# Kernel optimization log

Measured on AMD Instinct MI355X. Metric: run time of the kernel, lower is better.

## Reference

```python
import jax, jax.numpy as jnp
import numpy as np

N = 100000          # nodes
F_IN = 500          # num_features
HID = 256           # hidden
C = 40              # out_classes
E = 2302585         # ~ N*ln(N)*ec, doubled (both directions) in spar_samp
ALPHA0 = 0.1        # att[0][0] = alpha*(1-alpha)**0


def setup_inputs() -> dict:
    key = jax.random.key(0)
    ks = jax.random.split(key, 8)
    x = jax.random.normal(ks[0], (N, F_IN), dtype=jnp.float32)
    W1 = jax.random.normal(ks[1], (F_IN, HID), dtype=jnp.float32) * (1.0 / np.sqrt(F_IN))
    b1 = jnp.zeros((HID,), dtype=jnp.float32)
    W2 = jax.random.normal(ks[2], (HID, C), dtype=jnp.float32) * (1.0 / np.sqrt(HID))
    b2 = jnp.zeros((C,), dtype=jnp.float32)
    edge_row = jax.random.randint(ks[3], (E,), 0, N, dtype=jnp.int64) if jax.config.jax_enable_x64 else jax.random.randint(ks[3], (E,), 0, N, dtype=jnp.int32)
    edge_col = jax.random.randint(ks[4], (E,), 0, N, dtype=edge_row.dtype)
    # sampled importance weights: deg^{-1/2}*deg^{-1/2}*(M/num_edgess) -> small positive floats
    edge_val = jax.random.uniform(ks[5], (E,), dtype=jnp.float32, minval=0.001, maxval=0.05)
    return {"x": x, "W1": W1, "b1": b1, "W2": W2, "b2": b2,
            "edge_row": edge_row, "edge_col": edge_col, "edge_val": edge_val}


def reference(x, W1, b1, W2, b2, edge_row, edge_col, edge_val):
    # eval mode: dropout is identity
    h = jax.nn.relu(x @ W1 + b1)          # [N, HID]
    h = h @ W2 + b2                       # [N, C]
    # sparse propagation: out[r] += val * h[c]  (scatter-add SpMM)
    msg = edge_val[:, None] * h[edge_col]            # [E, C] gather
    agg = jax.ops.segment_sum(msg, edge_row, num_segments=N)  # [N, C]
    out = h * ALPHA0 + agg
    return jax.nn.log_softmax(out, axis=1)
```

## Files before the change

kernel.cpp:

```cpp
#include <hip/hip_runtime.h>
#include <hip/hip_bf16.h>


#define N_NODES 100000
#define F_IN    500
#define HID     256
#define C_OUT   40
#define ALPHA0  0.1f

#define RPB     128
#define NBUCK   ((N_NODES + RPB - 1) / RPB)
#define NCH     320
#define SCAN_M  (NBUCK * NCH)
#define SCAN_CHUNK 2048
#define NBS     ((SCAN_M + SCAN_CHUNK - 1) / SCAN_CHUNK)

typedef short short8 __attribute__((ext_vector_type(8)));
typedef float f32x4  __attribute__((ext_vector_type(4)));

__device__ __forceinline__ short f2bf(float f) {
  union { float f; unsigned u; } x; x.f = f;
  unsigned r = x.u + 0x7fffu + ((x.u >> 16) & 1u);
  return (short)(r >> 16);
}
__device__ __forceinline__ float bf2f(short s) {
  union { unsigned u; float f; } x; x.u = ((unsigned)(unsigned short)s) << 16;
  return x.f;
}

__device__ __forceinline__ void lbar() {
  asm volatile("s_waitcnt lgkmcnt(0)" ::: "memory");
  __builtin_amdgcn_s_barrier();
}

__global__ __launch_bounds__(256) void k_pack_weights(
    const float* __restrict__ W1, const float* __restrict__ W2,
    short* __restrict__ W1S, short* __restrict__ W2T)
{
  int i = blockIdx.x * 256 + threadIdx.x;
  if (i < 16*256*32) {
    int kc  = i >> 13;
    int idx = i & 8191;
    int n   = idx >> 5;
    int kk  = idx & 31;
    int k   = kc*32 + kk;
    float v = (k < F_IN) ? W1[k*HID + n] : 0.f;
    W1S[i] = f2bf(v);
  } else {
    int j = i - 16*256*32;
    if (j < 48*256) {
      int n = j >> 8;
      int k = j & 255;
      float v = (n < C_OUT) ? W2[k*C_OUT + n] : 0.f;
      W2T[j] = f2bf(v);
    }
  }
}

__global__ __launch_bounds__(512, 4) void k_fused_mlp(
    const float* __restrict__ x, const float* __restrict__ b1v,
    const float* __restrict__ b2v,
    const short* __restrict__ W1S, const short* __restrict__ W2T,
    short* __restrict__ h2b)
{
  __shared__ __align__(16) char smem[65536];
  short (*Ab)[128][40] = (short(*)[128][40])smem;
  short (*Hl)[256]     = (short(*)[256])smem;

  const int tid  = threadIdx.x;
  const int w    = tid >> 6;
  const int lane = tid & 63;
  const int lr   = lane & 15;
  const int quad = lane >> 4;
  const int wr   = w >> 2;
  const int wc   = w & 3;
  const int row0 = blockIdx.x * 128;

  const int srow = tid >> 2;
  const int sseg = tid & 3;
  const int grow = row0 + srow;
  const bool rok = grow < N_NODES;
  const float* ap = x + (size_t)grow * F_IN;

  f32x4 acc[4][4] = {};

  float rnxt[8];
  {
    int kb = sseg * 8;
    if (rok) {
      f32x4 u0 = *(const f32x4*)(ap + kb);
      f32x4 u1 = *(const f32x4*)(ap + kb + 4);
      #pragma unroll
      for (int j = 0; j < 4; ++j) { rnxt[j] = u0[j]; rnxt[4+j] = u1[j]; }
    } else {
      #pragma unroll
      for (int j = 0; j < 8; ++j) rnxt[j] = 0.f;
    }
    short tmp[8];
    #pragma unroll
    for (int j = 0; j < 8; ++j) tmp[j] = f2bf(rnxt[j]);
    *(short8*)&Ab[0][srow][sseg*8] = *(short8*)tmp;
  }

  const short* bbase = W1S + (wc*64 + lr)*32 + quad*8;

  for (int kc = 0; kc < 16; ++kc) {
    if (kc < 15) {
      int kb = (kc + 1)*32 + sseg*8;
      if (rok && kb + 8 <= F_IN) {
        f32x4 u0 = *(const f32x4*)(ap + kb);
        f32x4 u1 = *(const f32x4*)(ap + kb + 4);
        #pragma unroll
        for (int j = 0; j < 4; ++j) { rnxt[j] = u0[j]; rnxt[4+j] = u1[j]; }
      } else {
        #pragma unroll
        for (int j = 0; j < 8; ++j)
          rnxt[j] = (rok && kb + j < F_IN) ? ap[kb + j] : 0.f;
      }
    }
    lbar();

    short8 af[4], bf4[4];
    #pragma unroll
    for (int t = 0; t < 4; ++t)
      bf4[t] = *(const short8*)(bbase + kc*8192 + t*16*32);
    #pragma unroll
    for (int t = 0; t < 4; ++t)
      af[t] = *(const short8*)&Ab[kc & 1][wr*64 + t*16 + lr][quad*8];

    #pragma unroll
    for (int rt = 0; rt < 4; ++rt)
      #pragma unroll
      for (int ct = 0; ct < 4; ++ct)
        acc[rt][ct] = __builtin_amdgcn_mfma_f32_16x16x32_bf16(af[rt], bf4[ct], acc[rt][ct], 0, 0, 0);

    if (kc < 15) {
      short tmp[8];
      #pragma unroll
      for (int j = 0; j < 8; ++j) tmp[j] = f2bf(rnxt[j]);
      *(short8*)&Ab[(kc + 1) & 1][srow][sseg*8] = *(short8*)tmp;
    }
  }
  lbar();

  #pragma unroll
  for (int ct = 0; ct < 4; ++ct) {
    int col = wc*64 + ct*16 + lr;
    int cg = col >> 3, ci = col & 7;
    float bias = b1v[col];
    #pragma unroll
    for (int rt = 0; rt < 4; ++rt) {
      #pragma unroll
      for (int r = 0; r < 4; ++r) {
        int row = wr*64 + rt*16 + quad*4 + r;
        float v = fmaxf(acc[rt][ct][r] + bias, 0.f);
        Hl[row][((cg ^ (row & 31)) << 3) | ci] = f2bf(v);
      }
    }
  }
  lbar();

  f32x4 acc2[3] = {};
  const int arow = w*16 + lr;
  #pragma unroll
  for (int kc2 = 0; kc2 < 8; ++kc2) {
    int gg = kc2*4 + quad;
    short8 a2 = *(const short8*)&Hl[arow][(gg ^ (arow & 31)) << 3];
    #pragma unroll
    for (int nt = 0; nt < 3; ++nt) {
      short8 b2 = *(const short8*)(W2T + (nt*16 + lr)*256 + kc2*32 + quad*8);
      acc2[nt] = __builtin_amdgcn_mfma_f32_16x16x32_bf16(a2, b2, acc2[nt], 0, 0, 0);
    }
  }

  #pragma unroll
  for (int nt = 0; nt < 3; ++nt) {
    int col = nt*16 + lr;
    if (col < C_OUT) {
      float bias = b2v[col];
      #pragma unroll
      for (int r = 0; r < 4; ++r) {
        int row = row0 + w*16 + quad*4 + r;
        if (row < N_NODES)
          h2b[(long)row * C_OUT + col] = f2bf(acc2[nt][r] + bias);
      }
    }
  }
}

__global__ __launch_bounds__(256) void k_hist2(
    const int* __restrict__ erow, int* __restrict__ offs, int E, int CH)
{
  __shared__ int h[NBUCK];
  int tid = threadIdx.x, c = blockIdx.x;
  for (int b = tid; b < NBUCK; b += 256) h[b] = 0;
  __syncthreads();
  int e0 = c * CH, e1 = min(E, e0 + CH);
  for (int e = e0 + tid; e < e1; e += 256)
    atomicAdd(&h[erow[e] >> 7], 1);
  __syncthreads();
  for (int b = tid; b < NBUCK; b += 256) offs[b * NCH + c] = h[b];
}

__global__ __launch_bounds__(256) void k_scan1(
    int* __restrict__ offs, int* __restrict__ bsums)
{
  __shared__ int sh[256];
  int tid = threadIdx.x;
  int base = blockIdx.x * SCAN_CHUNK + tid * 8;
  int d[8];
  #pragma unroll
  for (int k = 0; k < 8; ++k)
    d[k] = (base + k < SCAN_M) ? offs[base + k] : 0;
  int s = 0;
  #pragma unroll
  for (int k = 0; k < 8; ++k) s += d[k];
  sh[tid] = s;
  __syncthreads();
  for (int o = 1; o < 256; o <<= 1) {
    int v = (tid >= o) ? sh[tid - o] : 0;
    __syncthreads();
    if (tid >= o) sh[tid] += v;
    __syncthreads();
  }
  int run = sh[tid] - s;
  #pragma unroll
  for (int k = 0; k < 8; ++k) {
    if (base + k < SCAN_M) offs[base + k] = run;
    run += d[k];
  }
  if (tid == 255) bsums[blockIdx.x] = sh[255];
}

__global__ __launch_bounds__(256) void k_scan2(int* __restrict__ bsums) {
  __shared__ int sh[256];
  int tid = threadIdx.x;
  int v = (tid < NBS) ? bsums[tid] : 0;
  sh[tid] = v;
  __syncthreads();
  for (int o = 1; o < 256; o <<= 1) {
    int u = (tid >= o) ? sh[tid - o] : 0;
    __syncthreads();
    if (tid >= o) sh[tid] += u;
    __syncthreads();
  }
  if (tid < NBS) bsums[tid] = sh[tid] - v;
}

__global__ __launch_bounds__(256) void k_scan3(
    int* __restrict__ offs, const int* __restrict__ bsums)
{
  int i = blockIdx.x * 256 + threadIdx.x;
  if (i < SCAN_M) offs[i] += bsums[i >> 11];
}

__global__ __launch_bounds__(256) void k_split(
    const int* __restrict__ erow, const int* __restrict__ ecol,
    const float* __restrict__ eval, const int* __restrict__ offs,
    int2* __restrict__ sorted, int E, int CH)
{
  __shared__ int cur[NBUCK];
  int tid = threadIdx.x, c = blockIdx.x;
  for (int b = tid; b < NBUCK; b += 256) cur[b] = offs[b * NCH + c];
  __syncthreads();
  int e0 = c * CH, e1 = min(E, e0 + CH);
  for (int e = e0 + tid; e < e1; e += 256) {
    int r = erow[e];
    int b = r >> 7;
    int pos = atomicAdd(&cur[b], 1);
    int2 cv;
    cv.x = ecol[e] | ((r & 127) << 17);
    cv.y = __float_as_int(eval[e]);
    sorted[pos] = cv;
  }
}

__global__ __launch_bounds__(256) void k_csr(
    const int* __restrict__ offs, const int2* __restrict__ sorted,
    int2* __restrict__ sorted2, int* __restrict__ row_offs, int E)
{
  __shared__ int hist[RPB];
  __shared__ int scn[RPB];
  int tid = threadIdx.x, b = blockIdx.x;
  int start = offs[b * NCH];
  int end   = (b + 1 < NBUCK) ? offs[(b + 1) * NCH] : E;

  if (tid < RPB) hist[tid] = 0;
  __syncthreads();
  for (int e = start + tid; e < end; e += 256)
    atomicAdd(&hist[((unsigned)sorted[e].x) >> 17], 1);
  __syncthreads();
  if (tid < RPB) scn[tid] = hist[tid];
  __syncthreads();
  for (int o = 1; o < RPB; o <<= 1) {
    int v = (tid >= o && tid < RPB) ? scn[tid - o] : 0;
    __syncthreads();
    if (tid >= o && tid < RPB) scn[tid] += v;
    __syncthreads();
  }
  if (tid < RPB) {
    int excl = scn[tid] - hist[tid];
    int row = b * RPB + tid;
    if (row < N_NODES) row_offs[row] = start + excl;
    hist[tid] = excl;
  }
  __syncthreads();
  for (int e = start + tid; e < end; e += 256) {
    int2 cv = sorted[e];
    int rl = ((unsigned)cv.x) >> 17;
    int pos = start + atomicAdd(&hist[rl], 1);
    sorted2[pos] = cv;
  }
  if (b == 0 && tid == 0) row_offs[N_NODES] = E;
}

__global__ __launch_bounds__(256) void k_spmm_lsm(
    const int* __restrict__ row_offs, const int2* __restrict__ sorted2,
    const short* __restrict__ h2b, float* __restrict__ out)
{
  int row  = blockIdx.x * 4 + (threadIdx.x >> 6);
  int lane = threadIdx.x & 63;
  if (row >= N_NODES) return;

  float acc = 0.f;
  if (lane < C_OUT) acc = ALPHA0 * bf2f(h2b[(long)row * C_OUT + lane]);

  int e   = row_offs[row];
  int end = row_offs[row + 1];
  for (; e + 3 < end; e += 4) {
    int2 cv0 = sorted2[e];
    int2 cv1 = sorted2[e + 1];
    int2 cv2 = sorted2[e + 2];
    int2 cv3 = sorted2[e + 3];
    int c0 = cv0.x & 0x1FFFF, c1 = cv1.x & 0x1FFFF;
    int c2 = cv2.x & 0x1FFFF, c3 = cv3.x & 0x1FFFF;
    if (lane < C_OUT) {
      float g0 = bf2f(h2b[(long)c0 * C_OUT + lane]);
      float g1 = bf2f(h2b[(long)c1 * C_OUT + lane]);
      float g2 = bf2f(h2b[(long)c2 * C_OUT + lane]);
      float g3 = bf2f(h2b[(long)c3 * C_OUT + lane]);
      acc += __int_as_float(cv0.y) * g0;
      acc += __int_as_float(cv1.y) * g1;
      acc += __int_as_float(cv2.y) * g2;
      acc += __int_as_float(cv3.y) * g3;
    }
  }
  for (; e < end; ++e) {
    int2 cv = sorted2[e];
    int c0 = cv.x & 0x1FFFF;
    if (lane < C_OUT)
      acc += __int_as_float(cv.y) * bf2f(h2b[(long)c0 * C_OUT + lane]);
  }

  float m = (lane < C_OUT) ? acc : -INFINITY;
  #pragma unroll
  for (int o = 32; o > 0; o >>= 1) m = fmaxf(m, __shfl_xor(m, o));
  float ev = (lane < C_OUT) ? __expf(acc - m) : 0.f;
  float s = ev;
  #pragma unroll
  for (int o = 32; o > 0; o >>= 1) s += __shfl_xor(s, o);
  if (lane < C_OUT) out[(long)row * C_OUT + lane] = acc - m - __logf(s);
}

extern "C" void kernel_launch(void* const* d_in, const int* in_sizes, int n_in,
                              void* d_out, int out_size, void* d_ws, size_t ws_size,
                              hipStream_t stream) {
  const float* x    = (const float*)d_in[0];
  const float* W1   = (const float*)d_in[1];
  const float* b1   = (const float*)d_in[2];
  const float* W2   = (const float*)d_in[3];
  const float* b2   = (const float*)d_in[4];
  const int*   erow = (const int*)d_in[5];
  const int*   ecol = (const int*)d_in[6];
  const float* eval = (const float*)d_in[7];
  const int E  = in_sizes[5];
  const int CH = (E + NCH - 1) / NCH;

  char* p = (char*)d_ws;
  short* h2b      = (short*)p;  p += (size_t)N_NODES * C_OUT * 2;
  short* W1S      = (short*)p;  p += (size_t)16*256*32 * 2;
  short* W2T      = (short*)p;  p += (size_t)48*256 * 2;
  int*   offs     = (int*)p;    p += (size_t)SCAN_M * 4;
  int*   bsums    = (int*)p;    p += 256 * 4;
  int*   row_offs = (int*)p;    p += (size_t)(N_NODES + 4) * 4;
  int2*  sorted   = (int2*)p;   p += (size_t)E * 8;
  int2*  sorted2  = (int2*)p;
  float* out = (float*)d_out;

  k_pack_weights<<<(16*256*32 + 48*256 + 255)/256, 256, 0, stream>>>(W1, W2, W1S, W2T);
  k_fused_mlp<<<(N_NODES + 127)/128, 512, 0, stream>>>(x, b1, b2, W1S, W2T, h2b);
  k_hist2<<<NCH, 256, 0, stream>>>(erow, offs, E, CH);
  k_scan1<<<NBS, 256, 0, stream>>>(offs, bsums);
  k_scan2<<<1, 256, 0, stream>>>(bsums);
  k_scan3<<<(SCAN_M + 255)/256, 256, 0, stream>>>(offs, bsums);
  k_split<<<NCH, 256, 0, stream>>>(erow, ecol, eval, offs, sorted, E, CH);
  k_csr<<<NBUCK, 256, 0, stream>>>(offs, sorted, sorted2, row_offs, E);
  k_spmm_lsm<<<(N_NODES + 3)/4, 256, 0, stream>>>(row_offs, sorted2, h2b, out);
}
```

Baseline: 551.8 us.

## Stream x tiles via async global_load_lds pipeline and pad h2 rows to 64

The fused MLP now loads fp32 x tiles straight into LDS with global_load_lds in a 4-stage ring buffer, using a swizzled layout. It converts them to bf16 with packed cvt instructions at fragment-read time, replacing the register-staged load, convert and store double buffer. Separately, the h2 intermediate is padded to a 64-element row stride with zeroed tail columns, so SpMM gathers are 128-byte aligned and need no lane predicate. This trades more LDS traffic (fp32 in LDS) and a larger h2 buffer for overlapped loads and aligned gathers. Tail handling of K=500 relies on clamped addresses and the padded W1S zeros.

After: 546.8 us. No clear change (-0.9%).

```diff
diff --git a/kernel.cpp b/kernel.cpp
--- a/kernel.cpp
+++ b/kernel.cpp
@@ -7,6 +7,7 @@
 #define HID     256
 #define C_OUT   40
 #define ALPHA0  0.1f
+#define H2STRIDE 64
 
 #define RPB     128
 #define NBUCK   ((N_NODES + RPB - 1) / RPB)
@@ -27,10 +28,19 @@
   union { unsigned u; float f; } x; x.u = ((unsigned)(unsigned short)s) << 16;
   return x.f;
 }
-
+__device__ __forceinline__ unsigned cvtpk(float lo, float hi) {
+  unsigned r;
+  asm("v_cvt_pk_bf16_f32 %0, %1, %2" : "=v"(r) : "v"(lo), "v"(hi));
+  return r;
+}
 __device__ __forceinline__ void lbar() {
   asm volatile("s_waitcnt lgkmcnt(0)" ::: "memory");
   __builtin_amdgcn_s_barrier();
+}
+__device__ __forceinline__ void gll16(const float* g, const char* l) {
+  __builtin_amdgcn_global_load_lds(
+      (const __attribute__((address_space(1))) void*)g,
+      (__attribute__((address_space(3))) void*)l, 16, 0, 0);
 }
 
 __global__ __launch_bounds__(256) void k_pack_weights(
@@ -64,8 +74,7 @@
     short* __restrict__ h2b)
 {
   __shared__ __align__(16) char smem[65536];
-  short (*Ab)[128][40] = (short(*)[128][40])smem;
-  short (*Hl)[256]     = (short(*)[256])smem;
+  short (*Hl)[256] = (short(*)[256])smem;
 
   const int tid  = threadIdx.x;
   const int w    = tid >> 6;
@@ -76,70 +85,71 @@
   const int wc   = w & 3;
   const int row0 = blockIdx.x * 128;
 
-  const int srow = tid >> 2;
-  const int sseg = tid & 3;
-  const int grow = row0 + srow;
-  const bool rok = grow < N_NODES;
-  const float* ap = x + (size_t)grow * F_IN;
+  const int s_rl0 = (w*2)*8 + (lane>>3);
+  const int s_rl1 = (w*2+1)*8 + (lane>>3);
+  const int ksw   = ((lane&7) ^ ((lane>>3)&7)) * 4;
+  const float* gp0 = x + (size_t)min(row0 + s_rl0, N_NODES-1) * F_IN;
+  const float* gp1 = x + (size_t)min(row0 + s_rl1, N_NODES-1) * F_IN;
+  const char* l0 = smem + (w*2)*1024;
+  const char* l1 = smem + (w*2+1)*1024;
 
   f32x4 acc[4][4] = {};
 
-  float rnxt[8];
-  {
-    int kb = sseg * 8;
-    if (rok) {
-      f32x4 u0 = *(const f32x4*)(ap + kb);
-      f32x4 u1 = *(const f32x4*)(ap + kb + 4);
-      #pragma unroll
-      for (int j = 0; j < 4; ++j) { rnxt[j] = u0[j]; rnxt[4+j] = u1[j]; }
-    } else {
-      #pragma unroll
-      for (int j = 0; j < 8; ++j) rnxt[j] = 0.f;
-    }
-    short tmp[8];
-    #pragma unroll
-    for (int j = 0; j < 8; ++j) tmp[j] = f2bf(rnxt[j]);
-    *(short8*)&Ab[0][srow][sseg*8] = *(short8*)tmp;
+  #pragma unroll
+  for (int p = 0; p < 2; ++p) {
+    int kb = p*32 + ksw;
+    const float* a0 = (kb + 4 <= F_IN) ? gp0 + kb : x;
+    const float* a1 = (kb + 4 <= F_IN) ? gp1 + kb : x;
+    gll16(a0, l0 + p*16384);
+    gll16(a1, l1 + p*16384);
   }
 
   const short* bbase = W1S + (wc*64 + lr)*32 + quad*8;
-
+  const int m2 = lr & 7;
+
+  #pragma unroll
   for (int kc = 0; kc < 16; ++kc) {
-    if (kc < 15) {
-      int kb = (kc + 1)*32 + sseg*8;
-      if (rok && kb + 8 <= F_IN) {
-        f32x4 u0 = *(const f32x4*)(ap + kb);
-        f32x4 u1 = *(const f32x4*)(ap + kb + 4);
-        #pragma unroll
-        for (int j = 0; j < 4; ++j) { rnxt[j] = u0[j]; rnxt[4+j] = u1[j]; }
-      } else {
-        #pragma unroll
-        for (int j = 0; j < 8; ++j)
-          rnxt[j] = (rok && kb + j < F_IN) ? ap[kb + j] : 0.f;
-      }
-    }
-    lbar();
-
-    short8 af[4], bf4[4];
+    short8 bf4[4];
     #pragma unroll
     for (int t = 0; t < 4; ++t)
       bf4[t] = *(const short8*)(bbase + kc*8192 + t*16*32);
-    #pragma unroll
-    for (int t = 0; t < 4; ++t)
-      af[t] = *(const short8*)&Ab[kc & 1][wr*64 + t*16 + lr][quad*8];
+    __builtin_amdgcn_sched_barrier(0);
+
+    if (kc < 14) {
+      int kb = (kc+2)*32 + ksw;
+      const float* a0 = (kb + 4 <= F_IN) ? gp0 + kb : x;
+      const float* a1 = (kb + 4 <= F_IN) ? gp1 + kb : x;
+      gll16(a0, l0 + ((kc+2)&3)*16384);
+      gll16(a1, l1 + ((kc+2)&3)*16384);
+      __builtin_amdgcn_sched_barrier(0);
+      asm volatile("s_waitcnt vmcnt(8)" ::: "memory");
+    } else if (kc == 14) {
+      asm volatile("s_waitcnt vmcnt(6)" ::: "memory");
+    } else {
+      asm volatile("s_waitcnt vmcnt(4)" ::: "memory");
+    }
+    __builtin_amdgcn_s_barrier();
+
+    const char* Abase = smem + (kc & 3)*16384;
+    short8 af[4];
+    #pragma unroll
+    for (int t = 0; t < 4; ++t) {
+      int rl = wr*64 + t*16 + lr;
+      f32x4 u0 = *(const f32x4*)(Abase + rl*128 + (((quad*2  ) ^ m2) << 4));
+      f32x4 u1 = *(const f32x4*)(Abase + rl*128 + (((quad*2+1) ^ m2) << 4));
+      union { unsigned u[4]; short8 s; } pk;
+      pk.u[0] = cvtpk(u0[0], u0[1]);
+      pk.u[1] = cvtpk(u0[2], u0[3]);
+      pk.u[2] = cvtpk(u1[0], u1[1]);
+      pk.u[3] = cvtpk(u1[2], u1[3]);
+      af[t] = pk.s;
+    }
 
     #pragma unroll
     for (int rt = 0; rt < 4; ++rt)
       #pragma unroll
       for (int ct = 0; ct < 4; ++ct)
         acc[rt][ct] = __builtin_amdgcn_mfma_f32_16x16x32_bf16(af[rt], bf4[ct], acc[rt][ct], 0, 0, 0);
-
-    if (kc < 15) {
-      short tmp[8];
-      #pragma unroll
-      for (int j = 0; j < 8; ++j) tmp[j] = f2bf(rnxt[j]);
-      *(short8*)&Ab[(kc + 1) & 1][srow][sseg*8] = *(short8*)tmp;
-    }
   }
   lbar();
 
@@ -176,14 +186,22 @@
   #pragma unroll
   for (int nt = 0; nt < 3; ++nt) {
     int col = nt*16 + lr;
-    if (col < C_OUT) {
-      float bias = b2v[col];
-      #pragma unroll
-      for (int r = 0; r < 4; ++r) {
-        int row = row0 + w*16 + quad*4 + r;
-        if (row < N_NODES)
-          h2b[(long)row * C_OUT + col] = f2bf(acc2[nt][r] + bias);
+    float bias = (col < C_OUT) ? b2v[col] : 0.f;
+    #pragma unroll
+    for (int r = 0; r < 4; ++r) {
+      int row = row0 + w*16 + quad*4 + r;
+      if (row < N_NODES) {
+        float v = (col < C_OUT) ? (acc2[nt][r] + bias) : 0.f;
+        h2b[(long)row * H2STRIDE + col] = f2bf(v);
       }
+    }
+  }
+  {
+    int col = 48 + lr;
+    #pragma unroll
+    for (int r = 0; r < 4; ++r) {
+      int row = row0 + w*16 + quad*4 + r;
+      if (row < N_NODES) h2b[(long)row * H2STRIDE + col] = 0;
     }
   }
 }
@@ -322,8 +340,7 @@
   int lane = threadIdx.x & 63;
   if (row >= N_NODES) return;
 
-  float acc = 0.f;
-  if (lane < C_OUT) acc = ALPHA0 * bf2f(h2b[(long)row * C_OUT + lane]);
+  float acc = ALPHA0 * bf2f(h2b[(long)row * H2STRIDE + lane]);
 
   int e   = row_offs[row];
   int end = row_offs[row + 1];
@@ -334,22 +351,19 @@
     int2 cv3 = sorted2[e + 3];
     int c0 = cv0.x & 0x1FFFF, c1 = cv1.x & 0x1FFFF;
     int c2 = cv2.x & 0x1FFFF, c3 = cv3.x & 0x1FFFF;
-    if (lane < C_OUT) {
-      float g0 = bf2f(h2b[(long)c0 * C_OUT + lane]);
-      float g1 = bf2f(h2b[(long)c1 * C_OUT + lane]);
-      float g2 = bf2f(h2b[(long)c2 * C_OUT + lane]);
-      float g3 = bf2f(h2b[(long)c3 * C_OUT + lane]);
-      acc += __int_as_float(cv0.y) * g0;
-      acc += __int_as_float(cv1.y) * g1;
-      acc += __int_as_float(cv2.y) * g2;
-      acc += __int_as_float(cv3.y) * g3;
-    }
+    float g0 = bf2f(h2b[(long)c0 * H2STRIDE + lane]);
+    float g1 = bf2f(h2b[(long)c1 * H2STRIDE + lane]);
+    float g2 = bf2f(h2b[(long)c2 * H2STRIDE + lane]);
+    float g3 = bf2f(h2b[(long)c3 * H2STRIDE + lane]);
+    acc += __int_as_float(cv0.y) * g0;
+    acc += __int_as_float(cv1.y) * g1;
+    acc += __int_as_float(cv2.y) * g2;
+    acc += __int_as_float(cv3.y) * g3;
   }
   for (; e < end; ++e) {
     int2 cv = sorted2[e];
     int c0 = cv.x & 0x1FFFF;
-    if (lane < C_OUT)
-      acc += __int_as_float(cv.y) * bf2f(h2b[(long)c0 * C_OUT + lane]);
+    acc += __int_as_float(cv.y) * bf2f(h2b[(long)c0 * H2STRIDE + lane]);
   }
 
   float m = (lane < C_OUT) ? acc : -INFINITY;
@@ -377,7 +391,7 @@
   const int CH = (E + NCH - 1) / NCH;
 
   char* p = (char*)d_ws;
-  short* h2b      = (short*)p;  p += (size_t)N_NODES * C_OUT * 2;
+  short* h2b      = (short*)p;  p += (size_t)N_NODES * H2STRIDE * 2;
   short* W1S      = (short*)p;  p += (size_t)16*256*32 * 2;
   short* W2T      = (short*)p;  p += (size_t)48*256 * 2;
   int*   offs     = (int*)p;    p += (size_t)SCAN_M * 4;
```
